# Kernel tuning notes

Measured on AMD Instinct MI355X. Metric: run time of the kernel, lower is better.

The kernel has to match this reference:

```python
import jax, jax.numpy as jnp
import numpy as np

D = 1024
H = 16
HD = D // H
EPS = 1e-6


def rms_norm(x, w):
    # x: [..., hd]; compute in float32 like the torch module
    xf = x.astype(jnp.float32)
    rms = jnp.sqrt(jnp.mean(xf * xf, axis=-1, keepdims=True) + EPS)
    return (xf / rms * w.astype(jnp.float32)).astype(x.dtype)


def setup_inputs() -> dict:
    key = jax.random.key(0)
    ks = jax.random.split(key, 6)
    B, S = 2, 2048
    x = jax.random.normal(ks[0], (B, S, D), dtype=jnp.float32)
    Wqkv = jax.random.normal(ks[1], (3 * D, D), dtype=jnp.float32) * (1.0 / np.sqrt(D))
    bqkv = jax.random.normal(ks[2], (3 * D,), dtype=jnp.float32) * 0.02
    Wproj = jax.random.normal(ks[3], (D, D), dtype=jnp.float32) * (1.0 / np.sqrt(D))
    bproj = jax.random.normal(ks[4], (D,), dtype=jnp.float32) * 0.02
    qn_w = jnp.ones((HD,), dtype=jnp.float32)
    kn_w = jnp.ones((HD,), dtype=jnp.float32)
    return {"x": x, "Wqkv": Wqkv, "bqkv": bqkv, "Wproj": Wproj, "bproj": bproj,
            "qn_w": qn_w, "kn_w": kn_w}


def reference(x, Wqkv, bqkv, Wproj, bproj, qn_w, kn_w):
    B, S, _ = x.shape
    # QKV projection: torch Linear is x @ W.T + b
    qkv = x @ Wqkv.T + bqkv                     # [B, S, 3D]
    qkv = qkv.reshape(B, S, 3, H, HD)
    q, k, v = qkv[:, :, 0], qkv[:, :, 1], qkv[:, :, 2]   # each [B, S, H, hd]
    q = rms_norm(q, qn_w)
    k = rms_norm(k, kn_w)
    # move heads forward: [B, H, S, hd]
    q = q.transpose(0, 2, 1, 3)
    k = k.transpose(0, 2, 1, 3)
    v = v.transpose(0, 2, 1, 3)
    scale = 1.0 / np.sqrt(HD)
    scores = jnp.einsum('bhsd,bhtd->bhst', q, k) * scale   # [B, H, S, S] (math backend)
    attn = jax.nn.softmax(scores, axis=-1)
    out = jnp.einsum('bhst,bhtd->bhsd', attn, v)            # [B, H, S, hd]
    out = out.transpose(0, 2, 1, 3).reshape(B, S, D)
    return out @ Wproj.T + bproj
```

## Files before the change

kernel.cpp:

```cpp
#include <hip/hip_runtime.h>
#include <hip/hip_bf16.h>
#include <math.h>

#define D_MODEL 1024
#define NH 16
#define HD 64
#define SEQ 2048
#define BATCH 2
#define NTOK (BATCH*SEQ)

typedef short bf16x8 __attribute__((ext_vector_type(8)));
typedef short s4 __attribute__((ext_vector_type(4)));
typedef float f32x4 __attribute__((ext_vector_type(4)));
typedef unsigned short us4 __attribute__((ext_vector_type(4)));

#define MFMA(a,b,c) __builtin_amdgcn_mfma_f32_16x16x32_bf16(a,b,c,0,0,0)

union bfu { __hip_bfloat16 b; unsigned short u; };
__device__ __forceinline__ unsigned short f2b(float f){ bfu t; t.b = __float2bfloat16(f); return t.u; }
__device__ __forceinline__ float b2f(unsigned short u){ bfu t; t.u = u; return __bfloat162float(t.b); }
__device__ __forceinline__ unsigned short f2bf(float f){
    unsigned int u = __float_as_uint(f);
    u += 0x7FFFu + ((u >> 16) & 1u);
    return (unsigned short)(u >> 16);
}

__device__ __forceinline__ void g2l16(const unsigned short* g, unsigned short* l){
    __builtin_amdgcn_global_load_lds(
        (const __attribute__((address_space(1))) unsigned int*)g,
        (__attribute__((address_space(3))) unsigned int*)l, 16, 0, 0);
}

#define OFF_X   128L
#define OFF_WQ  (OFF_X  + 4194304L)
#define OFF_BQ  (OFF_WQ + 3145728L)
#define OFF_WP  (OFF_BQ + 3072L)
#define OFF_BP  (OFF_WP + 1048576L)
#define OFF_QN  (OFF_BP + 1024L)
#define OFF_KN  (OFF_QN + 64L)
#define OFF_Q   (OFF_KN + 64L)
#define OFF_K   (OFF_Q  + 4194304L)
#define OFF_V   (OFF_K  + 4194304L)
#define OFF_A   (OFF_V  + 4194304L)


__global__ __launch_bounds__(256) void detect_kernel(
    const unsigned int* __restrict__ xraw, int* __restrict__ cnt)
{
    int i = blockIdx.x*256 + threadIdx.x;
    uint4 v = ((const uint4*)xraw)[i];
    unsigned int w[4] = {v.x, v.y, v.z, v.w};
    int local = 0;
    #pragma unroll
    for (int j=0;j<4;j++){
        local += ((w[j] & 0x7F80u) >= 0x4800u);
        local += (((w[j]>>16) & 0x7F80u) >= 0x4800u);
    }
    if (local) atomicAdd(cnt, local);
}

__global__ __launch_bounds__(256) void convert_kernel(
    const void* __restrict__ x,  const void* __restrict__ wq,
    const void* __restrict__ bq, const void* __restrict__ wp,
    const void* __restrict__ bp, const void* __restrict__ qn,
    const void* __restrict__ kn, unsigned short* __restrict__ ws,
    const int* __restrict__ cntp)
{
    const int flag = (*cntp > 256);
    long i = (long)blockIdx.x*blockDim.x + threadIdx.x;
    const long stride = (long)gridDim.x*blockDim.x;
    const long NCH = 2098208L;
    for (; i < NCH; i += stride){
        long j = i; const void* src; long off;
        if (j < 1048576L)                  { src = x;  off = OFF_X;  }
        else if ((j -= 1048576L) < 786432L){ src = wq; off = OFF_WQ; }
        else if ((j -= 786432L)  < 768L)   { src = bq; off = OFF_BQ; }
        else if ((j -= 768L)     < 262144L){ src = wp; off = OFF_WP; }
        else if ((j -= 262144L)  < 256L)   { src = bp; off = OFF_BP; }
        else if ((j -= 256L)     < 16L)    { src = qn; off = OFF_QN; }
        else      { j -= 16L;                src = kn; off = OFF_KN; }
        us4 o;
        if (flag){
            float4 v = ((const float4*)src)[j];
            o.x = f2b(v.x); o.y = f2b(v.y); o.z = f2b(v.z); o.w = f2b(v.w);
        } else {
            o = ((const us4*)src)[j];
        }
        *(us4*)(ws + off + j*4) = o;
    }
}

__global__ __launch_bounds__(256) void qkv_kernel(
    const unsigned short* __restrict__ x,
    const unsigned short* __restrict__ Wqkv,
    const unsigned short* __restrict__ bqkv,
    const unsigned short* __restrict__ qn_w,
    const unsigned short* __restrict__ kn_w,
    unsigned short* __restrict__ qbuf,
    unsigned short* __restrict__ kbuf,
    unsigned short* __restrict__ vbuf)
{
    __shared__ __align__(16) unsigned short tA[128*32];
    __shared__ __align__(16) unsigned short tB[128*32];
    const int tid  = threadIdx.x;
    const int w    = tid >> 6, lane = tid & 63, quad = lane >> 4, c = lane & 15;
    const int m0 = blockIdx.y*128, n0 = blockIdx.x*128;
    const int am = (w>>1)*64, bn = (w&1)*64;

    f32x4 acc[4][4];
    for (int mi=0;mi<4;mi++) for (int ni=0;ni<4;ni++) acc[mi][ni] = {0.f,0.f,0.f,0.f};

    const int i0 = tid, i1 = tid + 256;
    const long ga0 = (long)(m0 + (i0>>2))*D_MODEL + (i0&3)*8;
    const long ga1 = (long)(m0 + (i1>>2))*D_MODEL + (i1&3)*8;
    const long gb0 = (long)(n0 + (i0>>2))*D_MODEL + (i0&3)*8;
    const long gb1 = (long)(n0 + (i1>>2))*D_MODEL + (i1&3)*8;

    for (int k0=0;k0<D_MODEL;k0+=32){
        g2l16(x    + ga0 + k0, tA + i0*8);
        g2l16(x    + ga1 + k0, tA + i1*8);
        g2l16(Wqkv + gb0 + k0, tB + i0*8);
        g2l16(Wqkv + gb1 + k0, tB + i1*8);
        __syncthreads();
        bf16x8 a[4], b[4];
        for (int mi=0;mi<4;mi++) a[mi] = *(const bf16x8*)(tA + (am + mi*16 + c)*32 + quad*8);
        for (int ni=0;ni<4;ni++) b[ni] = *(const bf16x8*)(tB + (bn + ni*16 + c)*32 + quad*8);
        for (int mi=0;mi<4;mi++)
            for (int ni=0;ni<4;ni++)
                acc[mi][ni] = MFMA(a[mi], b[ni], acc[mi][ni]);
        __syncthreads();
    }

    const int nw = n0 + bn, mw = m0 + am;
    const int region = nw >> 10;
    const int h      = (nw & 1023) >> 6;
    float bias[4], wn[4];
    for (int ni=0;ni<4;ni++){
        bias[ni] = b2f(bqkv[nw + ni*16 + c]);
        wn[ni]   = 1.0f;
    }
    if (region==0) for (int ni=0;ni<4;ni++) wn[ni] = b2f(qn_w[ni*16+c]);
    if (region==1) for (int ni=0;ni<4;ni++) wn[ni] = b2f(kn_w[ni*16+c]);

    for (int mi=0;mi<4;mi++){
        for (int ni=0;ni<4;ni++)
            for (int r=0;r<4;r++) acc[mi][ni][r] += bias[ni];

        float scale_r[4];
        if (region < 2){
            for (int r=0;r<4;r++){
                float ss = 0.f;
                for (int ni=0;ni<4;ni++){ float v2 = acc[mi][ni][r]; ss += v2*v2; }
                ss += __shfl_xor(ss, 1, 64);
                ss += __shfl_xor(ss, 2, 64);
                ss += __shfl_xor(ss, 4, 64);
                ss += __shfl_xor(ss, 8, 64);
                scale_r[r] = rsqrtf(ss*(1.0f/64.0f) + 1e-6f);
            }
        } else {
            for (int r=0;r<4;r++) scale_r[r] = 1.0f;
        }

        for (int r=0;r<4;r++){
            int m = mw + mi*16 + quad*4 + r;
            int bidx = m >> 11, s = m & 2047;
            long bb = (long)(bidx*NH + h)*SEQ*HD;
            if (region == 0){
                long base = bb + (long)s*HD;
                for (int ni=0;ni<4;ni++)
                    qbuf[base + ni*16 + c] = f2bf(acc[mi][ni][r] * scale_r[r] * wn[ni]);
            } else if (region == 1){
                long tb = bb + (long)(s>>6)*4096;
                for (int ni=0;ni<4;ni++){
                    int d = ni*16 + c;
                    long idx = tb + (long)((s&63)*8 + ((d>>3) ^ (s&7)))*8 + (d&7);
                    kbuf[idx] = f2bf(acc[mi][ni][r] * scale_r[r] * wn[ni]);
                }
            } else {
                long tb = bb + (long)(s>>6)*4096;
                for (int ni=0;ni<4;ni++){
                    int d = ni*16 + c;
                    long idx = tb + (long)(d*8 + (((s>>3)&7) ^ (d&7)))*8 + (s&7);
                    vbuf[idx] = f2bf(acc[mi][ni][r]);
                }
            }
        }
    }
}

__global__ __launch_bounds__(256) void attn_kernel(
    const unsigned short* __restrict__ qbuf,
    const unsigned short* __restrict__ kts,
    const unsigned short* __restrict__ vts,
    unsigned short* __restrict__ abuf)
{
    const int tid = threadIdx.x, w = tid>>6, lane = tid&63, quad = lane>>4, c = lane&15;
    const int bh = blockIdx.y, qt = blockIdx.x;
    const unsigned short* qb = qbuf + (long)bh*SEQ*HD;
    const unsigned short* kb = kts + (long)bh*SEQ*HD;
    const unsigned short* vb = vts + (long)bh*SEQ*HD;
    const int qbase = qt*128 + w*32;
    const int cq = c & 7;

    __shared__ __align__(16) unsigned short KT[2][4096];
    __shared__ __align__(16) unsigned short VT[2][4096];
    __shared__ __align__(16) unsigned short P[4][2112];
    unsigned short* Pw = &P[w][0];

    bf16x8 aq[2][2];
    #pragma unroll
    for (int mi=0;mi<2;mi++)
        #pragma unroll
        for (int ks=0;ks<2;ks++)
            aq[mi][ks] = *(const bf16x8*)(qb + (long)(qbase + mi*16 + c)*HD + ks*32 + quad*8);

    f32x4 o[2][4];
    #pragma unroll
    for (int mi=0;mi<2;mi++)
        #pragma unroll
        for (int nt=0;nt<4;nt++) o[mi][nt] = {0.f,0.f,0.f,0.f};
    float l_loc[2] = {0.f, 0.f};

    auto stage = [&](const unsigned short* src, unsigned short* dst){
        g2l16(src + tid*8,        dst + tid*8);
        g2l16(src + 2048 + tid*8, dst + 2048 + tid*8);
    };

    stage(kb, KT[0]); stage(vb, VT[0]);
    __syncthreads();

    for (int kt2=0; kt2<SEQ/64; kt2++){
        const unsigned short* ktl = KT[kt2&1];
        const unsigned short* vtl = VT[kt2&1];
        if (kt2 < SEQ/64 - 1){
            stage(kb + (kt2+1)*4096, KT[(kt2&1)^1]);
            stage(vb + (kt2+1)*4096, VT[(kt2&1)^1]);
        }

        bf16x8 kf[4][2];
        #pragma unroll
        for (int mt=0;mt<4;mt++)
            #pragma unroll
            for (int ks=0;ks<2;ks++)
                kf[mt][ks] = *(const bf16x8*)(ktl + ((mt*16+c)*8 + ((ks*4+quad)^cq))*8);

        f32x4 z4[4][2];
        #pragma unroll
        for (int mt=0;mt<4;mt++)
            #pragma unroll
            for (int mi=0;mi<2;mi++){
                f32x4 t = {0.f,0.f,0.f,0.f};
                t = MFMA(kf[mt][0], aq[mi][0], t);
                t = MFMA(kf[mt][1], aq[mi][1], t);
                z4[mt][mi] = t;
            }

        #pragma unroll
        for (int mt=0;mt<4;mt++){
            const int key8 = mt*2 + (quad>>1);
            #pragma unroll
            for (int mi=0;mi<2;mi++){
                s4 pk;
                #pragma unroll
                for (int r=0;r<4;r++){
                    float p = exp2f(z4[mt][mi][r]*0.18033688f - 17.312340f);
                    l_loc[mi] += p;
                    pk[r] = (short)(__float_as_uint(p) >> 16);
                }
                *(s4*)(Pw + key8*264 + (mi*16+c)*8 + (quad&1)*4) = pk;
            }
        }

        #pragma unroll
        for (int ks=0;ks<2;ks++){
            bf16x8 bv[4];
            #pragma unroll
            for (int nt=0;nt<4;nt++)
                bv[nt] = *(const bf16x8*)(vtl + ((nt*16+c)*8 + ((ks*4+quad)^cq))*8);
            bf16x8 ap0 = *(const bf16x8*)(Pw + (ks*4+quad)*264 + c*8);
            bf16x8 ap1 = *(const bf16x8*)(Pw + (ks*4+quad)*264 + (16+c)*8);
            #pragma unroll
            for (int nt=0;nt<4;nt++){
                o[0][nt] = MFMA(ap0, bv[nt], o[0][nt]);
                o[1][nt] = MFMA(ap1, bv[nt], o[1][nt]);
            }
        }
        __syncthreads();
    }

    #pragma unroll
    for (int mi=0;mi<2;mi++){
        l_loc[mi] += __shfl_xor(l_loc[mi], 16, 64);
        l_loc[mi] += __shfl_xor(l_loc[mi], 32, 64);
    }

    const int b = bh >> 4, h = bh & 15;
    #pragma unroll
    for (int mi=0;mi<2;mi++)
        #pragma unroll
        for (int r=0;r<4;r++){
            float l = __shfl(l_loc[mi], quad*4 + r, 64);
            float inv = 1.0f / l;
            int s = qbase + mi*16 + quad*4 + r;
            long base = ((long)(b*SEQ + s)*NH + h)*HD;
            #pragma unroll
            for (int nt=0;nt<4;nt++)
                abuf[base + nt*16 + c] = f2bf(o[mi][nt][r]*inv);
        }
}

__global__ __launch_bounds__(256) void proj_kernel(
    const unsigned short* __restrict__ abuf,
    const unsigned short* __restrict__ Wp,
    const unsigned short* __restrict__ bp,
    void* __restrict__ outv,
    const int* __restrict__ cntp)
{
    __shared__ __align__(16) unsigned short tA[128*32];
    __shared__ __align__(16) unsigned short tB[64*32];
    const int tid  = threadIdx.x;
    const int w    = tid >> 6, lane = tid & 63, quad = lane >> 4, c = lane & 15;
    const int m0 = blockIdx.y*128, n0 = blockIdx.x*64;
    const int am = (w>>1)*64, bn = (w&1)*32;
    const int flag = (*cntp > 256);

    f32x4 acc[4][2];
    for (int mi=0;mi<4;mi++) for (int ni=0;ni<2;ni++) acc[mi][ni] = {0.f,0.f,0.f,0.f};

    const int i0 = tid, i1 = tid + 256;
    const long ga0 = (long)(m0 + (i0>>2))*D_MODEL + (i0&3)*8;
    const long ga1 = (long)(m0 + (i1>>2))*D_MODEL + (i1&3)*8;
    const long gb0 = (long)(n0 + (i0>>2))*D_MODEL + (i0&3)*8;

    for (int k0=0;k0<D_MODEL;k0+=32){
        g2l16(abuf + ga0 + k0, tA + i0*8);
        g2l16(abuf + ga1 + k0, tA + i1*8);
        g2l16(Wp   + gb0 + k0, tB + i0*8);
        __syncthreads();
        bf16x8 a[4], b[2];
        for (int mi=0;mi<4;mi++) a[mi] = *(const bf16x8*)(tA + (am + mi*16 + c)*32 + quad*8);
        for (int ni=0;ni<2;ni++) b[ni] = *(const bf16x8*)(tB + (bn + ni*16 + c)*32 + quad*8);
        for (int mi=0;mi<4;mi++)
            for (int ni=0;ni<2;ni++)
                acc[mi][ni] = MFMA(a[mi], b[ni], acc[mi][ni]);
        __syncthreads();
    }

    float bias[2];
    for (int ni=0;ni<2;ni++) bias[ni] = b2f(bp[n0 + bn + ni*16 + c]);

    for (int mi=0;mi<4;mi++)
        for (int r=0;r<4;r++){
            long m = m0 + am + mi*16 + quad*4 + r;
            for (int ni=0;ni<2;ni++){
                float val = acc[mi][ni][r] + bias[ni];
                long idx = m*D_MODEL + n0 + bn + ni*16 + c;
                if (flag) ((float*)outv)[idx] = val;
                else      ((unsigned short*)outv)[idx] = f2bf(val);
            }
        }
}

extern "C" void kernel_launch(void* const* d_in, const int* in_sizes, int n_in,
                              void* d_out, int out_size, void* d_ws, size_t ws_size,
                              hipStream_t stream)
{
    unsigned short* ws = (unsigned short*)d_ws;
    int* cnt = (int*)d_ws;

    hipMemsetAsync(cnt, 0, 4, stream);
    hipLaunchKernelGGL(detect_kernel, dim3(16), dim3(256), 0, stream,
                       (const unsigned int*)d_in[0], cnt);
    hipLaunchKernelGGL(convert_kernel, dim3(2048), dim3(256), 0, stream,
                       d_in[0], d_in[1], d_in[2], d_in[3], d_in[4], d_in[5], d_in[6],
                       ws, cnt);
    hipLaunchKernelGGL(qkv_kernel,  dim3(24,32), dim3(256), 0, stream,
                       ws+OFF_X, ws+OFF_WQ, ws+OFF_BQ, ws+OFF_QN, ws+OFF_KN,
                       ws+OFF_Q, ws+OFF_K, ws+OFF_V);
    hipLaunchKernelGGL(attn_kernel, dim3(16,32), dim3(256), 0, stream,
                       ws+OFF_Q, ws+OFF_K, ws+OFF_V, ws+OFF_A);
    hipLaunchKernelGGL(proj_kernel, dim3(16,32), dim3(256), 0, stream,
                       ws+OFF_A, ws+OFF_WP, ws+OFF_BP, d_out, cnt);
}
```

Baseline: 217.9 us.

## Halve attention query tile per block and compute row sums via MFMA

Each attention wave now handles 16 query rows instead of 32. Block tiles shrink to 64 queries, the grid doubles, and launch bounds request 4 blocks per SM to raise occupancy. The softmax denominator is accumulated with an extra MFMA against a ones vector instead of scalar adds and shuffles. Probability packing uses a byte-permute instruction. The aim is more parallel blocks and fewer registers. The cost is twice the K/V tile loads per query and less MFMA reuse of each K/V fragment.

Measured after the change: 219.5 us. No clear change (+0.7%).

```diff
diff --git a/kernel.cpp b/kernel.cpp
--- a/kernel.cpp
+++ b/kernel.cpp
@@ -188,7 +188,7 @@
     }
 }
 
-__global__ __launch_bounds__(256) void attn_kernel(
+__global__ __launch_bounds__(256, 4) void attn_kernel(
     const unsigned short* __restrict__ qbuf,
     const unsigned short* __restrict__ kts,
     const unsigned short* __restrict__ vts,
@@ -199,27 +199,27 @@
     const unsigned short* qb = qbuf + (long)bh*SEQ*HD;
     const unsigned short* kb = kts + (long)bh*SEQ*HD;
     const unsigned short* vb = vts + (long)bh*SEQ*HD;
-    const int qbase = qt*128 + w*32;
+    const int qbase = qt*64 + w*16;
     const int cq = c & 7;
 
     __shared__ __align__(16) unsigned short KT[2][4096];
     __shared__ __align__(16) unsigned short VT[2][4096];
-    __shared__ __align__(16) unsigned short P[4][2112];
+    __shared__ __align__(16) unsigned short P[4][1024];
     unsigned short* Pw = &P[w][0];
 
-    bf16x8 aq[2][2];
-    #pragma unroll
-    for (int mi=0;mi<2;mi++)
-        #pragma unroll
-        for (int ks=0;ks<2;ks++)
-            aq[mi][ks] = *(const bf16x8*)(qb + (long)(qbase + mi*16 + c)*HD + ks*32 + quad*8);
-
-    f32x4 o[2][4];
-    #pragma unroll
-    for (int mi=0;mi<2;mi++)
-        #pragma unroll
-        for (int nt=0;nt<4;nt++) o[mi][nt] = {0.f,0.f,0.f,0.f};
-    float l_loc[2] = {0.f, 0.f};
+    bf16x8 aq[2];
+    #pragma unroll
+    for (int ks=0;ks<2;ks++)
+        aq[ks] = *(const bf16x8*)(qb + (long)(qbase + c)*HD + ks*32 + quad*8);
+
+    bf16x8 onesf;
+    #pragma unroll
+    for (int j=0;j<8;j++) onesf[j] = (short)0x3F80;
+
+    f32x4 o[4], o4;
+    #pragma unroll
+    for (int nt=0;nt<4;nt++) o[nt] = {0.f,0.f,0.f,0.f};
+    o4 = {0.f,0.f,0.f,0.f};
 
     auto stage = [&](const unsigned short* src, unsigned short* dst){
         g2l16(src + tid*8,        dst + tid*8);
@@ -244,31 +244,26 @@
             for (int ks=0;ks<2;ks++)
                 kf[mt][ks] = *(const bf16x8*)(ktl + ((mt*16+c)*8 + ((ks*4+quad)^cq))*8);
 
-        f32x4 z4[4][2];
-        #pragma unroll
-        for (int mt=0;mt<4;mt++)
-            #pragma unroll
-            for (int mi=0;mi<2;mi++){
-                f32x4 t = {0.f,0.f,0.f,0.f};
-                t = MFMA(kf[mt][0], aq[mi][0], t);
-                t = MFMA(kf[mt][1], aq[mi][1], t);
-                z4[mt][mi] = t;
-            }
+        f32x4 z4[4];
+        #pragma unroll
+        for (int mt=0;mt<4;mt++){
+            f32x4 t = {0.f,0.f,0.f,0.f};
+            t = MFMA(kf[mt][0], aq[0], t);
+            t = MFMA(kf[mt][1], aq[1], t);
+            z4[mt] = t;
+        }
 
         #pragma unroll
         for (int mt=0;mt<4;mt++){
             const int key8 = mt*2 + (quad>>1);
-            #pragma unroll
-            for (int mi=0;mi<2;mi++){
-                s4 pk;
-                #pragma unroll
-                for (int r=0;r<4;r++){
-                    float p = exp2f(z4[mt][mi][r]*0.18033688f - 17.312340f);
-                    l_loc[mi] += p;
-                    pk[r] = (short)(__float_as_uint(p) >> 16);
-                }
-                *(s4*)(Pw + key8*264 + (mi*16+c)*8 + (quad&1)*4) = pk;
-            }
+            unsigned int u0 = __float_as_uint(exp2f(z4[mt][0]*0.18033688f - 17.312340f));
+            unsigned int u1 = __float_as_uint(exp2f(z4[mt][1]*0.18033688f - 17.312340f));
+            unsigned int u2 = __float_as_uint(exp2f(z4[mt][2]*0.18033688f - 17.312340f));
+            unsigned int u3 = __float_as_uint(exp2f(z4[mt][3]*0.18033688f - 17.312340f));
+            uint2 pk;
+            pk.x = __builtin_amdgcn_perm(u1, u0, 0x07060302u);
+            pk.y = __builtin_amdgcn_perm(u3, u2, 0x07060302u);
+            *(uint2*)(Pw + key8*128 + c*8 + (quad&1)*4) = pk;
         }
 
         #pragma unroll
@@ -277,36 +272,25 @@
             #pragma unroll
             for (int nt=0;nt<4;nt++)
                 bv[nt] = *(const bf16x8*)(vtl + ((nt*16+c)*8 + ((ks*4+quad)^cq))*8);
-            bf16x8 ap0 = *(const bf16x8*)(Pw + (ks*4+quad)*264 + c*8);
-            bf16x8 ap1 = *(const bf16x8*)(Pw + (ks*4+quad)*264 + (16+c)*8);
-            #pragma unroll
-            for (int nt=0;nt<4;nt++){
-                o[0][nt] = MFMA(ap0, bv[nt], o[0][nt]);
-                o[1][nt] = MFMA(ap1, bv[nt], o[1][nt]);
-            }
-        }
-        __syncthreads();
-    }
-
-    #pragma unroll
-    for (int mi=0;mi<2;mi++){
-        l_loc[mi] += __shfl_xor(l_loc[mi], 16, 64);
-        l_loc[mi] += __shfl_xor(l_loc[mi], 32, 64);
-    }
-
-    const int b = bh >> 4, h = bh & 15;
-    #pragma unroll
-    for (int mi=0;mi<2;mi++)
-        #pragma unroll
-        for (int r=0;r<4;r++){
-            float l = __shfl(l_loc[mi], quad*4 + r, 64);
-            float inv = 1.0f / l;
-            int s = qbase + mi*16 + quad*4 + r;
-            long base = ((long)(b*SEQ + s)*NH + h)*HD;
+            bf16x8 ap = *(const bf16x8*)(Pw + (ks*4+quad)*128 + c*8);
             #pragma unroll
             for (int nt=0;nt<4;nt++)
-                abuf[base + nt*16 + c] = f2bf(o[mi][nt][r]*inv);
-        }
+                o[nt] = MFMA(ap, bv[nt], o[nt]);
+            o4 = MFMA(ap, onesf, o4);
+        }
+        __syncthreads();
+    }
+
+    const int b = bh >> 4, h = bh & 15;
+    #pragma unroll
+    for (int r=0;r<4;r++){
+        float inv = 1.0f / o4[r];
+        int s = qbase + quad*4 + r;
+        long base = ((long)(b*SEQ + s)*NH + h)*HD;
+        #pragma unroll
+        for (int nt=0;nt<4;nt++)
+            abuf[base + nt*16 + c] = f2bf(o[nt][r]*inv);
+    }
 }
 
 __global__ __launch_bounds__(256) void proj_kernel(
@@ -377,7 +361,7 @@
     hipLaunchKernelGGL(qkv_kernel,  dim3(24,32), dim3(256), 0, stream,
                        ws+OFF_X, ws+OFF_WQ, ws+OFF_BQ, ws+OFF_QN, ws+OFF_KN,
                        ws+OFF_Q, ws+OFF_K, ws+OFF_V);
-    hipLaunchKernelGGL(attn_kernel, dim3(16,32), dim3(256), 0, stream,
+    hipLaunchKernelGGL(attn_kernel, dim3(32,32), dim3(256), 0, stream,
                        ws+OFF_Q, ws+OFF_K, ws+OFF_V, ws+OFF_A);
     hipLaunchKernelGGL(proj_kernel, dim3(16,32), dim3(256), 0, stream,
                        ws+OFF_A, ws+OFF_WP, ws+OFF_BP, d_out, cnt);
```
